# Performance work log

Hardware: AMD Instinct MI355X
Metric: run time of the kernel (lower is better)

The kernel has to match this reference:

```python
import jax, jax.numpy as jnp
import numpy as np
import math

B, S, D = 4, 2048, 1024
TAU = 0.5

def setup_inputs() -> dict:
    key = jax.random.key(0)
    ks = jax.random.split(key, 10)
    s = 1.0 / math.sqrt(D)
    return {
        "node_emb": jax.random.normal(ks[0], (B, S, D), jnp.float32),
        "label_emb": jax.random.normal(ks[1], (B, S, D), jnp.float32),
        "Wq": jax.random.uniform(ks[2], (D, D), jnp.float32, -s, s),
        "bq": jax.random.uniform(ks[3], (D,), jnp.float32, -s, s),
        "Wk": jax.random.uniform(ks[4], (D, D), jnp.float32, -s, s),
        "bk": jax.random.uniform(ks[5], (D,), jnp.float32, -s, s),
        "Wv": jax.random.uniform(ks[6], (D, D), jnp.float32, -s, s),
        "bv": jax.random.uniform(ks[7], (D,), jnp.float32, -s, s),
        "Wp": jax.random.uniform(ks[8], (D, D), jnp.float32, -s, s),
        "bp": jax.random.uniform(ks[9], (D,), jnp.float32, -s, s),
    }

def reference(node_emb, label_emb, Wq, bq, Wk, bk, Wv, bv, Wp, bp):
    # Q from label_emb; K, V from node_emb (torch Linear: x @ W.T + b)
    Q = label_emb @ Wq.T + bq          # [B, S, D]
    K = node_emb @ Wk.T + bk           # [B, S, D]
    V = node_emb @ Wv.T + bv           # [B, S, D]
    d = node_emb.shape[-1]
    score = jnp.einsum('bqd,bkd->bqk', Q, K) / jnp.sqrt(jnp.float32(d))
    # causal (lower-triangular) mask, masked_fill(-1e9) BEFORE the tau scale
    causal = jnp.tril(jnp.ones((score.shape[-2], score.shape[-1]), bool))
    score = jnp.where(causal[None, :, :], score, jnp.float32(-1e9))
    attn = jax.nn.softmax(score * TAU, axis=-1)  # [B, S, S]
    # proj_drop is Dropout(0.1); reference runs in eval mode (identity)
    z = jnp.einsum('bqk,bkd->bqd', attn, V)
    return z @ Wp.T + bp
```

## Files before the change

kernel.cpp:

```cpp
#include <hip/hip_runtime.h>
#include <hip/hip_bf16.h>
#include <stdint.h>

using bf16 = __hip_bfloat16;
typedef __bf16 bf16x8 __attribute__((ext_vector_type(8)));
typedef float f32x4 __attribute__((ext_vector_type(4)));
typedef unsigned short u16x8 __attribute__((ext_vector_type(8)));
typedef unsigned short u16x4 __attribute__((ext_vector_type(4)));

#define AS1 __attribute__((address_space(1)))
#define AS3 __attribute__((address_space(3)))

__device__ inline unsigned short f2b(float f) {
    union { __hip_bfloat16 h; unsigned short u; } cv;
    cv.h = __float2bfloat16(f);
    return cv.u;
}

__global__ __launch_bounds__(256) void cvt6(
    const float* __restrict__ i0, const float* __restrict__ i1,
    const float* __restrict__ i2, const float* __restrict__ i3,
    const float* __restrict__ i4, const float* __restrict__ i5,
    u16x8* __restrict__ o0, u16x8* __restrict__ o1,
    u16x8* __restrict__ o2, u16x8* __restrict__ o3,
    u16x8* __restrict__ o4, u16x8* __restrict__ o5,
    long nbig, long nsmall)
{
    const int y = blockIdx.y;
    const float* in = y == 0 ? i0 : (y == 1 ? i1 : (y == 2 ? i2 : (y == 3 ? i3 : (y == 4 ? i4 : i5))));
    u16x8* out = y == 0 ? o0 : (y == 1 ? o1 : (y == 2 ? o2 : (y == 3 ? o3 : (y == 4 ? o4 : o5))));
    const long n8 = (y < 2) ? nbig : nsmall;
    long i = (long)blockIdx.x * blockDim.x + threadIdx.x;
    const long stride = (long)gridDim.x * blockDim.x;
    const float4* in4 = (const float4*)in;
    for (; i < n8; i += stride) {
        float4 x = in4[2 * i], z = in4[2 * i + 1];
        u16x8 o;
        o[0] = f2b(x.x); o[1] = f2b(x.y); o[2] = f2b(x.z); o[3] = f2b(x.w);
        o[4] = f2b(z.x); o[5] = f2b(z.y); o[6] = f2b(z.z); o[7] = f2b(z.w);
        out[i] = o;
    }
}

template <typename T> __device__ inline void storev(T* p, float v);
template <> __device__ inline void storev<float>(float* p, float v) { *p = v; }
template <> __device__ inline void storev<bf16>(bf16* p, float v) { *p = __float2bfloat16(v); }

template <typename OutT, int MODE>
__global__ __launch_bounds__(512, 2) void gemmX(
    const bf16* __restrict__ A0, const bf16* __restrict__ A1,
    const bf16* __restrict__ B0p, const bf16* __restrict__ B1p,
    OutT* __restrict__ C0, OutT* __restrict__ C1,
    const float* __restrict__ bias0, const float* __restrict__ bias1,
    float scale, int lda, int ldb, int ldc, int Kdim,
    long sA, long sB, long sC)
{
    __shared__ __align__(16) char lds[131072];

    const int nwg = gridDim.x;
    const int bid = blockIdx.x;
    const int s = (nwg & 7) ? bid : ((bid & 7) * (nwg >> 3) + (bid >> 3));

    int bm, ccol0, rowB0, seg = 0, bn_s = 0, zidx = 0;
    const bf16 *A, *B;
    OutT* C;
    const float* bias = nullptr;

    if constexpr (MODE == 0) {
        bm = s >> 3; const int bnl = s & 7; seg = bnl >> 2;
        A = A0; B = B0p; rowB0 = bnl * 256;
        C = seg ? C1 : C0; bias = seg ? bias1 : bias0;
        ccol0 = (bnl & 3) * 256;
    } else if constexpr (MODE == 1) {
        seg = s >> 7; const int r = s & 127; bm = r >> 2; const int bn = r & 3;
        A = seg ? A1 : A0; B = seg ? B1p : B0p;
        C = seg ? C1 : C0; bias = seg ? nullptr : bias0;
        rowB0 = bn * 256; ccol0 = bn * 256;
    } else {
        const int z = s / 36, f = s % 36;
        int m = 0;
        while ((m + 1) * (m + 2) / 2 <= f) ++m;
        bm = m; const int bn = f - m * (m + 1) / 2;
        bn_s = bn; zidx = z;
        A = A0 + (long)z * sA; B = B0p + (long)z * sB; C = C0 + (long)z * sC;
        rowB0 = bn * 256; ccol0 = bn * 256;
    }

    const int KT = Kdim >> 6;
    const int NIT = KT >> 1;

    const int tid = threadIdx.x;
    const int lane = tid & 63;
    const int w = tid >> 6;
    const int wm = w >> 2;
    const int wn = w & 3;

    const int rowA0 = bm * 256;

    const int rr  = tid >> 3;
    const int lch = (tid & 7) ^ (rr & 7);
    const bf16* gAt = A + (long)(rowA0 + rr) * lda + lch * 8;
    const bf16* gBt = B + (long)(rowB0 + rr) * ldb + lch * 8;

#define LA(b) (lds + (b) * 65536)
#define LB(b) (lds + 32768 + (b) * 65536)

    auto SG2 = [&](const bf16* g, int ld, char* dst) {
        __builtin_amdgcn_global_load_lds((const AS1 void*)g,
            (AS3 void*)(dst + tid * 16), 16, 0, 0);
        __builtin_amdgcn_global_load_lds((const AS1 void*)(g + (long)64 * ld),
            (AS3 void*)(dst + 8192 + tid * 16), 16, 0, 0);
    };
    auto ST_A = [&](int kt, int half, int b) {
        SG2(gAt + (long)kt * 64 + (long)half * 128 * lda, lda, LA(b) + half * 16384);
    };
    auto ST_B = [&](int kt, int half, int b) {
        SG2(gBt + (long)kt * 64 + (long)half * 128 * ldb, ldb, LB(b) + half * 16384);
    };

    const int abase = (wm * 128 + (lane & 15)) * 128;
    const int bbase = (wn * 64 + (lane & 15)) * 128;
    const int cc0 = (((lane >> 4) << 4)) ^ ((lane & 7) << 4);
    const int cc1 = cc0 ^ 64;

#define RAF(b, mh, mi, kk) (*(const bf16x8*)(LA(b) + abase + (mh)*8192 + (mi)*2048 + ((kk) ? cc1 : cc0)))
#define RBF(b, ni, kk)     (*(const bf16x8*)(LB(b) + bbase + (ni)*2048 + ((kk) ? cc1 : cc0)))

    f32x4 acc[8][4] = {};
    bf16x8 ar[4][2], blo[2][2], bhi[2][2];

#define RD_A2(b, mh, MI0) { ar[MI0][0] = RAF(b, mh, MI0, 0); ar[MI0][1] = RAF(b, mh, MI0, 1); \
                            ar[(MI0)+1][0] = RAF(b, mh, (MI0)+1, 0); ar[(MI0)+1][1] = RAF(b, mh, (MI0)+1, 1); }
#define RD_BLO(b)   { blo[0][0] = RBF(b, 0, 0); blo[0][1] = RBF(b, 0, 1); blo[1][0] = RBF(b, 1, 0); blo[1][1] = RBF(b, 1, 1); }
#define RD_BHI(b)   { bhi[0][0] = RBF(b, 2, 0); bhi[0][1] = RBF(b, 2, 1); bhi[1][0] = RBF(b, 3, 0); bhi[1][1] = RBF(b, 3, 1); }

#define MQ1(MI, bb, MH, NB) { \
    f32x4 t0_ = acc[(MH)*4 + (MI)][(NB)]; \
    t0_ = __builtin_amdgcn_mfma_f32_16x16x32_bf16(ar[MI][0], bb[0][0], t0_, 0, 0, 0); \
    t0_ = __builtin_amdgcn_mfma_f32_16x16x32_bf16(ar[MI][1], bb[0][1], t0_, 0, 0, 0); \
    acc[(MH)*4 + (MI)][(NB)] = t0_; \
    f32x4 t1_ = acc[(MH)*4 + (MI)][(NB) + 1]; \
    t1_ = __builtin_amdgcn_mfma_f32_16x16x32_bf16(ar[MI][0], bb[1][0], t1_, 0, 0, 0); \
    t1_ = __builtin_amdgcn_mfma_f32_16x16x32_bf16(ar[MI][1], bb[1][1], t1_, 0, 0, 0); \
    acc[(MH)*4 + (MI)][(NB) + 1] = t1_; }

#define SCHEDB     __builtin_amdgcn_sched_barrier(0)
#define PRE_SYNC { asm volatile("s_waitcnt lgkmcnt(0)" ::: "memory"); __builtin_amdgcn_sched_barrier(0); \
                   __builtin_amdgcn_s_barrier(); __builtin_amdgcn_sched_barrier(0); }

    auto BAR = [&]() { __builtin_amdgcn_s_barrier(); SCHEDB; };
    auto PRIO1 = [&]() { __builtin_amdgcn_s_setprio(1); };
    auto PRIO0 = [&]() { __builtin_amdgcn_s_setprio(0); };

    ST_A(0, 0, 0); ST_A(0, 1, 0); ST_B(0, 0, 0); ST_B(0, 1, 0);
    ST_B(1, 0, 1); ST_B(1, 1, 1);
    asm volatile("s_waitcnt vmcnt(4)" ::: "memory");
    BAR();
    RD_BLO(0); RD_A2(0, 0, 0); RD_A2(0, 0, 2);

    for (int i = 0; i < NIT; ++i) {
        const int t0 = 2 * i;
        const bool last = (i == NIT - 1);

        ST_A(t0 + 1, 0, 1);
        PRE_SYNC; PRIO1();
        RD_BHI(0);
        MQ1(0, blo, 0, 0); MQ1(1, blo, 0, 0); MQ1(2, blo, 0, 0); MQ1(3, blo, 0, 0);
        PRIO0();

        ST_A(t0 + 1, 1, 1);
        PRE_SYNC; PRIO1();
        MQ1(0, bhi, 0, 2); MQ1(1, bhi, 0, 2); MQ1(2, bhi, 0, 2); MQ1(3, bhi, 0, 2);
        RD_A2(0, 1, 0); RD_A2(0, 1, 2);
        PRIO0();

        if (!last) ST_B(t0 + 2, 0, 0);
        PRE_SYNC; PRIO1();
        MQ1(0, bhi, 1, 2); MQ1(1, bhi, 1, 2); MQ1(2, bhi, 1, 2); MQ1(3, bhi, 1, 2);
        PRIO0();

        if (!last) { ST_B(t0 + 2, 1, 0);
                     asm volatile("s_waitcnt vmcnt(4)" ::: "memory"); }
        else       { asm volatile("s_waitcnt vmcnt(0)" ::: "memory"); }
        PRE_SYNC; PRIO1();
        MQ1(0, blo, 1, 0); MQ1(1, blo, 1, 0); MQ1(2, blo, 1, 0); MQ1(3, blo, 1, 0);
        RD_BLO(1); RD_A2(1, 0, 0); RD_A2(1, 0, 2);
        PRIO0();

        if (!last) ST_A(t0 + 2, 0, 0);
        PRE_SYNC; PRIO1();
        RD_BHI(1);
        MQ1(0, blo, 0, 0); MQ1(1, blo, 0, 0); MQ1(2, blo, 0, 0); MQ1(3, blo, 0, 0);
        PRIO0();

        if (!last) ST_A(t0 + 2, 1, 0);
        PRE_SYNC; PRIO1();
        MQ1(0, bhi, 0, 2); MQ1(1, bhi, 0, 2); MQ1(2, bhi, 0, 2); MQ1(3, bhi, 0, 2);
        RD_A2(1, 1, 0); RD_A2(1, 1, 2);
        PRIO0();

        if (!last) ST_B(t0 + 3, 0, 1);
        PRE_SYNC; PRIO1();
        MQ1(0, bhi, 1, 2); MQ1(1, bhi, 1, 2); MQ1(2, bhi, 1, 2); MQ1(3, bhi, 1, 2);
        PRIO0();

        if (!last) { ST_B(t0 + 3, 1, 1);
                     asm volatile("s_waitcnt vmcnt(4)" ::: "memory"); }
        PRE_SYNC; PRIO1();
        MQ1(0, blo, 1, 0); MQ1(1, blo, 1, 0); MQ1(2, blo, 1, 0); MQ1(3, blo, 1, 0);
        if (!last) { RD_BLO(0); RD_A2(0, 0, 0); RD_A2(0, 0, 2); }
        PRIO0();
    }

    char* tw = lds + w * 16384;
    if constexpr (MODE == 2) {
        const int q = lane >> 4, t = lane & 15;
        const bool diag = (bm == bn_s);
#pragma unroll
        for (int mi = 0; mi < 8; ++mi)
#pragma unroll
            for (int ni = 0; ni < 4; ++ni)
#pragma unroll
                for (int j = 0; j < 4; ++j) {
                    float e = __expf(acc[mi][ni][j] * scale);
                    if (diag) {
                        const int rl = wm * 128 + mi * 16 + q * 4 + j;
                        const int cl = wn * 64 + t + ni * 16;
                        if (cl > rl) e = 0.f;
                    }
                    e = __bfloat162float(__float2bfloat16(e));
                    acc[mi][ni][j] = e;
                }
        float* part = (float*)C1 + ((((long)zidx * 8 + bm) * 32) + bn_s * 4 + wn) * 256;
#pragma unroll
        for (int mi = 0; mi < 8; ++mi) {
            float rs0 = acc[mi][0][0] + acc[mi][1][0] + acc[mi][2][0] + acc[mi][3][0];
            float rs1 = acc[mi][0][1] + acc[mi][1][1] + acc[mi][2][1] + acc[mi][3][1];
            float rs2 = acc[mi][0][2] + acc[mi][1][2] + acc[mi][2][2] + acc[mi][3][2];
            float rs3 = acc[mi][0][3] + acc[mi][1][3] + acc[mi][2][3] + acc[mi][3][3];
#pragma unroll
            for (int d = 1; d < 16; d <<= 1) {
                rs0 += __shfl_xor(rs0, d); rs1 += __shfl_xor(rs1, d);
                rs2 += __shfl_xor(rs2, d); rs3 += __shfl_xor(rs3, d);
            }
            if (t == mi) {
                float4 o; o.x = rs0; o.y = rs1; o.z = rs2; o.w = rs3;
                *(float4*)(part + wm * 128 + mi * 16 + q * 4) = o;
            }
        }
    }
    if (MODE == 1 && seg == 1) {
#pragma unroll
        for (int ni = 0; ni < 4; ++ni) {
            const int cl = ni * 16 + (lane & 15);
            const int sw = 8 * (cl & 7);
#pragma unroll
            for (int mi = 0; mi < 8; ++mi) {
                const int rlb = mi * 16 + ((lane >> 4) << 2);
                u16x4 o;
                o[0] = f2b(acc[mi][ni][0]); o[1] = f2b(acc[mi][ni][1]);
                o[2] = f2b(acc[mi][ni][2]); o[3] = f2b(acc[mi][ni][3]);
                *(u16x4*)(tw + cl * 256 + 2 * (rlb ^ sw)) = o;
            }
        }
        asm volatile("s_waitcnt lgkmcnt(0)" ::: "memory");
        __builtin_amdgcn_sched_barrier(0);
        const int m0 = rowA0 + wm * 128;
        const int z2 = m0 >> 11, mr = m0 & 2047;
        bf16* CT = (bf16*)C + (long)z2 * 2097152 + (long)(ccol0 + wn * 64 + lane) * 2048 + mr;
        const char* tr = tw + lane * 256;
        const int sw2 = lane & 7;
#pragma unroll
        for (int rb = 0; rb < 16; ++rb) {
            u16x8 v = *(const u16x8*)(tr + 16 * (rb ^ sw2));
            *(u16x8*)(CT + 8 * rb) = v;
        }
    } else {
        const float sc2 = (MODE == 2) ? 1.0f : scale;
        const int q = lane >> 4, t = lane & 15;
        const int c0 = ccol0 + wn * 64 + t;
#pragma unroll
        for (int mi = 0; mi < 8; ++mi) {
            char* tm = tw + mi * 2048;
#pragma unroll
            for (int ni = 0; ni < 4; ++ni) {
                const float bv = bias ? bias[c0 + ni * 16] : 0.0f;
                const int cb = (t + 16 * ni) * 2;
#pragma unroll
                for (int j = 0; j < 4; ++j) {
                    const int rl = q * 4 + j;
                    *(bf16*)(tm + rl * 128 + (cb ^ ((rl & 7) << 4))) =
                        __float2bfloat16(acc[mi][ni][j] * sc2 + bv);
                }
            }
        }
        asm volatile("s_waitcnt lgkmcnt(0)" ::: "memory");
        __builtin_amdgcn_sched_barrier(0);
        const int rr2 = lane >> 2, chb = (lane & 3) * 2;
        const int gr0 = rowA0 + wm * 128;
        bf16* Cb = (bf16*)C;
        const int gcb = ccol0 + wn * 64;
#pragma unroll
        for (int mi = 0; mi < 8; ++mi) {
            const char* tm = tw + mi * 2048;
            const long gr = gr0 + mi * 16 + rr2;
#pragma unroll
            for (int k = 0; k < 2; ++k) {
                const int chunk = chb + k;
                u16x8 v = *(const u16x8*)(tm + rr2 * 128 + ((chunk << 4) ^ ((rr2 & 7) << 4)));
                *(u16x8*)(Cb + gr * (long)ldc + gcb + chunk * 8) = v;
            }
        }
    }
#undef RAF
#undef RBF
#undef RD_A2
#undef RD_BLO
#undef RD_BHI
#undef MQ1
#undef LA
#undef LB
}

__global__ __launch_bounds__(512, 2) void pv_bal(
    const bf16* __restrict__ P, const bf16* __restrict__ VT,
    const float* __restrict__ part, float* __restrict__ out,
    const float* __restrict__ bias)
{
    __shared__ __align__(16) char lds[99328];
    float* invl = (float*)(lds + 98304);

    const int nwg = gridDim.x;
    const int bid = blockIdx.x;
    const int s = (bid & 7) * (nwg >> 3) + (bid >> 3);
    const int z = s >> 6, r = s & 63;
    const int pr = r >> 3, bn = r & 7;
    const int bmA = pr, bmB = 15 - pr;

    const bf16* Pz = P + (long)z * 2048 * 2048;
    const bf16* Vz = VT + (long)z * 1024 * 2048;

    const int tid = threadIdx.x;
    const int lane = tid & 63;
    const int w = tid >> 6;
    const int wm = w >> 2, wn = w & 3;
    const int rr = tid >> 3;
    const int lch = (tid & 7) ^ (rr & 7);

    if (tid < 256) {
        const int half = tid >> 7, rloc = tid & 127;
        const int grow = (half ? bmB : bmA) * 128 + rloc;
        const int b256 = grow >> 8, rin = grow & 255;
        const float* pp = part + (((long)z * 8 + b256) * 32) * 256 + rin;
        const int n4 = 4 * (b256 + 1);
        float s0 = 0.f, s1 = 0.f, s2 = 0.f, s3 = 0.f;
        int b4 = 0;
        for (; b4 + 4 <= n4; b4 += 4) {
            s0 += pp[(long)b4 * 256];       s1 += pp[(long)(b4 + 1) * 256];
            s2 += pp[(long)(b4 + 2) * 256]; s3 += pp[(long)(b4 + 3) * 256];
        }
        for (; b4 < n4; ++b4) s0 += pp[(long)b4 * 256];
        invl[tid] = 1.0f / ((s0 + s1) + (s2 + s3));
    }

    const bf16* gBt = Vz + (long)(bn * 128 + rr) * 2048 + lch * 8;
    const bf16* gAtA = Pz + (long)(bmA * 128 + rr) * 2048 + lch * 8;
    const bf16* gAtB = Pz + (long)(bmB * 128 + rr) * 2048 + lch * 8;

    auto SG2 = [&](const bf16* g, char* dst) {
        __builtin_amdgcn_global_load_lds((const AS1 void*)g,
            (AS3 void*)(dst + tid * 16), 16, 0, 0);
        __builtin_amdgcn_global_load_lds((const AS1 void*)(g + (long)64 * 2048),
            (AS3 void*)(dst + 8192 + tid * 16), 16, 0, 0);
    };
    auto ST = [&](const bf16* gAt, int kt, int b) {
        SG2(gAt + (long)kt * 64, lds + b * 32768);
        SG2(gBt + (long)kt * 64, lds + b * 32768 + 16384);
    };

    const int abase0 = (wm * 64 + (lane & 15)) * 128;
    const int bbase0 = 16384 + (wn * 32 + (lane & 15)) * 128;
    const int cc0 = ((lane >> 4) << 4) ^ ((lane & 7) << 4);
    const int cc1 = cc0 ^ 64;

    f32x4 acc[4][2];
    bf16x8 ar[4][2], br[2][2];

    auto RDF = [&](int t) {
        const char* base = lds + (t % 3) * 32768;
#pragma unroll
        for (int mi = 0; mi < 4; ++mi) {
            ar[mi][0] = *(const bf16x8*)(base + abase0 + mi * 2048 + cc0);
            ar[mi][1] = *(const bf16x8*)(base + abase0 + mi * 2048 + cc1);
        }
#pragma unroll
        for (int ni = 0; ni < 2; ++ni) {
            br[ni][0] = *(const bf16x8*)(base + bbase0 + ni * 2048 + cc0);
            br[ni][1] = *(const bf16x8*)(base + bbase0 + ni * 2048 + cc1);
        }
    };
    auto MFMA16 = [&]() {
#pragma unroll
        for (int mi = 0; mi < 4; ++mi)
#pragma unroll
            for (int ni = 0; ni < 2; ++ni) {
                f32x4 t_ = acc[mi][ni];
                t_ = __builtin_amdgcn_mfma_f32_16x16x32_bf16(ar[mi][0], br[ni][0], t_, 0, 0, 0);
                t_ = __builtin_amdgcn_mfma_f32_16x16x32_bf16(ar[mi][1], br[ni][1], t_, 0, 0, 0);
                acc[mi][ni] = t_;
            }
    };
    auto ZERO = [&]() {
#pragma unroll
        for (int mi = 0; mi < 4; ++mi)
#pragma unroll
            for (int ni = 0; ni < 2; ++ni) acc[mi][ni] = f32x4{0.f, 0.f, 0.f, 0.f};
    };
    auto tile_pass = [&](const bf16* gAt, int KT) {
        RDF(0);
        for (int t = 0; t < KT; ++t) {
            if (t + 2 < KT) {
                ST(gAt, t + 2, (t + 2) % 3);
                asm volatile("s_waitcnt vmcnt(4)" ::: "memory");
            } else if (t + 1 < KT) {
                asm volatile("s_waitcnt vmcnt(0)" ::: "memory");
            }
            asm volatile("s_waitcnt lgkmcnt(0)" ::: "memory");
            __builtin_amdgcn_sched_barrier(0);
            __builtin_amdgcn_s_barrier();
            __builtin_amdgcn_sched_barrier(0);
            __builtin_amdgcn_s_setprio(1);
            MFMA16();
            if (t + 1 < KT) RDF(t + 1);
            __builtin_amdgcn_s_setprio(0);
        }
    };
    auto epi = [&](int bm, int invoff) {
        const int q = lane >> 4, t16 = lane & 15;
        const int c0 = bn * 128 + wn * 32 + t16;
        float* op = out + ((long)z * 2048 + (long)bm * 128) * 1024;
#pragma unroll
        for (int mi = 0; mi < 4; ++mi)
#pragma unroll
            for (int j = 0; j < 4; ++j) {
                const int rl = wm * 64 + mi * 16 + q * 4 + j;
                const float iv = invl[invoff + rl];
#pragma unroll
                for (int ni = 0; ni < 2; ++ni) {
                    const int c = c0 + ni * 16;
                    op[(long)rl * 1024 + c] = acc[mi][ni][j] * iv + bias[c];
                }
            }
    };

    const int KTA = 2 * (bmA + 1), KTB = 2 * (bmB + 1);

    ST(gAtA, 0, 0); ST(gAtA, 1, 1);
    asm volatile("s_waitcnt vmcnt(4)" ::: "memory");
    __builtin_amdgcn_s_barrier();
    __builtin_amdgcn_sched_barrier(0);
    ZERO();
    tile_pass(gAtA, KTA);

    ST(gAtB, 0, 0); ST(gAtB, 1, 1);
    epi(bmA, 0);
    asm volatile("s_waitcnt vmcnt(0)" ::: "memory");
    __builtin_amdgcn_s_barrier();
    __builtin_amdgcn_sched_barrier(0);
    ZERO();
    tile_pass(gAtB, KTB);
    epi(bmB, 128);
}

extern "C" void kernel_launch(void* const* d_in, const int* in_sizes, int n_in,
                              void* d_out, int out_size, void* d_ws, size_t ws_size,
                              hipStream_t stream) {
    const int B = 4, S = 2048, D = 1024;
    const long MD = (long)B * S * D;
    const float scale = 0.5f / 32.0f;

    const float* node  = (const float*)d_in[0];
    const float* label = (const float*)d_in[1];
    const float* Wq = (const float*)d_in[2];
    const float* bq = (const float*)d_in[3];
    const float* Wk = (const float*)d_in[4];
    const float* bk = (const float*)d_in[5];
    const float* Wv = (const float*)d_in[6];
    const float* bv = (const float*)d_in[7];
    const float* Wp = (const float*)d_in[8];
    const float* bp = (const float*)d_in[9];
    float* out = (float*)d_out;

    char* ws = (char*)d_ws;
    bf16* nodeb  = (bf16*)(ws);
    bf16* VTb    = nodeb;
    bf16* labelb = (bf16*)(ws + 16777216);
    bf16* Wqb = (bf16*)(ws + 33554432);
    bf16* Wkb = (bf16*)(ws + 35651584);
    bf16* Wvb = (bf16*)(ws + 37748736);
    bf16* Wpb = (bf16*)(ws + 39845888);
    bf16* Qb  = (bf16*)(ws + 41943040);
    bf16* Kb  = (bf16*)(ws + 58720256);
    bf16* Vb  = (bf16*)(ws + 75497472);
    float* partial = (float*)(ws + 75497472);
    bf16* SP  = (bf16*)(ws + 92274688);
    if (ws_size < 125829120UL) return;

    cvt6<<<dim3(512, 6), 256, 0, stream>>>(
        node, label, Wq, Wk, Wv, Wp,
        (u16x8*)nodeb, (u16x8*)labelb, (u16x8*)Wqb, (u16x8*)Wkb, (u16x8*)Wvb, (u16x8*)Wpb,
        MD / 8, (long)D * D / 8);

    gemmX<bf16, 0><<<256, 512, 0, stream>>>(
        nodeb, nullptr, Wkb, nullptr, Kb, Vb, bk, bv,
        1.0f, D, D, D, D, 0, 0, 0);

    gemmX<bf16, 1><<<256, 512, 0, stream>>>(
        labelb, Vb, Wqb, Wpb, Qb, VTb, bq, nullptr,
        1.0f, D, D, D, D, 0, 0, 0);

    gemmX<bf16, 2><<<144, 512, 0, stream>>>(
        Qb, nullptr, Kb, (bf16*)nullptr, SP, (bf16*)partial, nullptr, nullptr,
        scale, D, D, S, D, (long)S * D, (long)S * D, (long)S * S);

    pv_bal<<<256, 512, 0, stream>>>(SP, VTb, partial, out, bp);
}
```

Baseline: 153.4 us.

## Double-buffer GEMM fragment registers and drop per-phase lgkmcnt waits

Restructures the GEMM main loop's LDS-to-register schedule. A fragments now use separate even and odd register sets, and B-low fragments are double-buffered across k-tiles. The explicit lgkmcnt(0) waits before each barrier are removed, so LDS reads can overlap the MFMA phases and waits are left to the compiler. This raises VGPR pressure and relies on the compiler inserting correct waits; B-high fragments are no longer double-buffered, so the reordering has to keep reads ahead of the async global-to-LDS overwrites.

```diff
diff --git a/kernel.cpp b/kernel.cpp
--- a/kernel.cpp
+++ b/kernel.cpp
@@ -127,89 +127,78 @@
 #define RBF(b, ni, kk)     (*(const bf16x8*)(LB(b) + bbase + (ni)*2048 + ((kk) ? cc1 : cc0)))
 
     f32x4 acc[8][4] = {};
-    bf16x8 ar[4][2], blo[2][2], bhi[2][2];
-
-#define RD_A2(b, mh, MI0) { ar[MI0][0] = RAF(b, mh, MI0, 0); ar[MI0][1] = RAF(b, mh, MI0, 1); \
-                            ar[(MI0)+1][0] = RAF(b, mh, (MI0)+1, 0); ar[(MI0)+1][1] = RAF(b, mh, (MI0)+1, 1); }
-#define RD_BLO(b)   { blo[0][0] = RBF(b, 0, 0); blo[0][1] = RBF(b, 0, 1); blo[1][0] = RBF(b, 1, 0); blo[1][1] = RBF(b, 1, 1); }
-#define RD_BHI(b)   { bhi[0][0] = RBF(b, 2, 0); bhi[0][1] = RBF(b, 2, 1); bhi[1][0] = RBF(b, 3, 0); bhi[1][1] = RBF(b, 3, 1); }
-
-#define MQ1(MI, bb, MH, NB) { \
-    f32x4 t0_ = acc[(MH)*4 + (MI)][(NB)]; \
-    t0_ = __builtin_amdgcn_mfma_f32_16x16x32_bf16(ar[MI][0], bb[0][0], t0_, 0, 0, 0); \
-    t0_ = __builtin_amdgcn_mfma_f32_16x16x32_bf16(ar[MI][1], bb[0][1], t0_, 0, 0, 0); \
-    acc[(MH)*4 + (MI)][(NB)] = t0_; \
-    f32x4 t1_ = acc[(MH)*4 + (MI)][(NB) + 1]; \
-    t1_ = __builtin_amdgcn_mfma_f32_16x16x32_bf16(ar[MI][0], bb[1][0], t1_, 0, 0, 0); \
-    t1_ = __builtin_amdgcn_mfma_f32_16x16x32_bf16(ar[MI][1], bb[1][1], t1_, 0, 0, 0); \
-    acc[(MH)*4 + (MI)][(NB) + 1] = t1_; }
-
-#define SCHEDB     __builtin_amdgcn_sched_barrier(0)
-#define PRE_SYNC { asm volatile("s_waitcnt lgkmcnt(0)" ::: "memory"); __builtin_amdgcn_sched_barrier(0); \
-                   __builtin_amdgcn_s_barrier(); __builtin_amdgcn_sched_barrier(0); }
-
-    auto BAR = [&]() { __builtin_amdgcn_s_barrier(); SCHEDB; };
+    bf16x8 arE[4][2], arO[4][2], blA[2][2], blB[2][2], bh[2][2];
+
+#define RD_AE(b) { _Pragma("unroll") for (int mi = 0; mi < 4; ++mi) { arE[mi][0] = RAF(b, 0, mi, 0); arE[mi][1] = RAF(b, 0, mi, 1); } }
+#define RD_AO(b) { _Pragma("unroll") for (int mi = 0; mi < 4; ++mi) { arO[mi][0] = RAF(b, 1, mi, 0); arO[mi][1] = RAF(b, 1, mi, 1); } }
+#define RD_BLX(b, dst) { dst[0][0] = RBF(b, 0, 0); dst[0][1] = RBF(b, 0, 1); dst[1][0] = RBF(b, 1, 0); dst[1][1] = RBF(b, 1, 1); }
+#define RD_BHX(b)      { bh[0][0] = RBF(b, 2, 0); bh[0][1] = RBF(b, 2, 1); bh[1][0] = RBF(b, 3, 0); bh[1][1] = RBF(b, 3, 1); }
+
+#define MQX(ASET, BSET, MH, NB) { \
+    _Pragma("unroll") \
+    for (int mi = 0; mi < 4; ++mi) { \
+        f32x4 t0_ = acc[(MH)*4 + mi][(NB)]; \
+        t0_ = __builtin_amdgcn_mfma_f32_16x16x32_bf16(ASET[mi][0], BSET[0][0], t0_, 0, 0, 0); \
+        t0_ = __builtin_amdgcn_mfma_f32_16x16x32_bf16(ASET[mi][1], BSET[0][1], t0_, 0, 0, 0); \
+        acc[(MH)*4 + mi][(NB)] = t0_; \
+        f32x4 t1_ = acc[(MH)*4 + mi][(NB) + 1]; \
+        t1_ = __builtin_amdgcn_mfma_f32_16x16x32_bf16(ASET[mi][0], BSET[1][0], t1_, 0, 0, 0); \
+        t1_ = __builtin_amdgcn_mfma_f32_16x16x32_bf16(ASET[mi][1], BSET[1][1], t1_, 0, 0, 0); \
+        acc[(MH)*4 + mi][(NB) + 1] = t1_; } }
+
+#define SCHEDB __builtin_amdgcn_sched_barrier(0)
+#define BARX   { __builtin_amdgcn_s_barrier(); SCHEDB; }
+#define VM4    { asm volatile("s_waitcnt vmcnt(4)" ::: "memory"); SCHEDB; }
+#define VM0    { asm volatile("s_waitcnt vmcnt(0)" ::: "memory"); SCHEDB; }
+
     auto PRIO1 = [&]() { __builtin_amdgcn_s_setprio(1); };
     auto PRIO0 = [&]() { __builtin_amdgcn_s_setprio(0); };
 
     ST_A(0, 0, 0); ST_A(0, 1, 0); ST_B(0, 0, 0); ST_B(0, 1, 0);
     ST_B(1, 0, 1); ST_B(1, 1, 1);
-    asm volatile("s_waitcnt vmcnt(4)" ::: "memory");
-    BAR();
-    RD_BLO(0); RD_A2(0, 0, 0); RD_A2(0, 0, 2);
+    VM4; BARX;
+    RD_AE(0); RD_BLX(0, blA); RD_BHX(0);
 
     for (int i = 0; i < NIT; ++i) {
         const int t0 = 2 * i;
         const bool last = (i == NIT - 1);
 
         ST_A(t0 + 1, 0, 1);
-        PRE_SYNC; PRIO1();
-        RD_BHI(0);
-        MQ1(0, blo, 0, 0); MQ1(1, blo, 0, 0); MQ1(2, blo, 0, 0); MQ1(3, blo, 0, 0);
-        PRIO0();
+        BARX;
+        RD_AO(0);
+        PRIO1(); MQX(arE, blA, 0, 0); PRIO0();
 
         ST_A(t0 + 1, 1, 1);
-        PRE_SYNC; PRIO1();
-        MQ1(0, bhi, 0, 2); MQ1(1, bhi, 0, 2); MQ1(2, bhi, 0, 2); MQ1(3, bhi, 0, 2);
-        RD_A2(0, 1, 0); RD_A2(0, 1, 2);
-        PRIO0();
-
+        BARX;
+        PRIO1(); MQX(arE, bh, 0, 2); PRIO0();
+
+        BARX;
         if (!last) ST_B(t0 + 2, 0, 0);
-        PRE_SYNC; PRIO1();
-        MQ1(0, bhi, 1, 2); MQ1(1, bhi, 1, 2); MQ1(2, bhi, 1, 2); MQ1(3, bhi, 1, 2);
-        PRIO0();
-
-        if (!last) { ST_B(t0 + 2, 1, 0);
-                     asm volatile("s_waitcnt vmcnt(4)" ::: "memory"); }
-        else       { asm volatile("s_waitcnt vmcnt(0)" ::: "memory"); }
-        PRE_SYNC; PRIO1();
-        MQ1(0, blo, 1, 0); MQ1(1, blo, 1, 0); MQ1(2, blo, 1, 0); MQ1(3, blo, 1, 0);
-        RD_BLO(1); RD_A2(1, 0, 0); RD_A2(1, 0, 2);
-        PRIO0();
+        PRIO1(); MQX(arO, bh, 1, 2); PRIO0();
+
+        if (!last) { ST_B(t0 + 2, 1, 0); VM4; }
+        else       { VM0; }
+        BARX;
+        RD_AE(1); RD_BLX(1, blB); RD_BHX(1);
+        PRIO1(); MQX(arO, blA, 1, 0); PRIO0();
 
         if (!last) ST_A(t0 + 2, 0, 0);
-        PRE_SYNC; PRIO1();
-        RD_BHI(1);
-        MQ1(0, blo, 0, 0); MQ1(1, blo, 0, 0); MQ1(2, blo, 0, 0); MQ1(3, blo, 0, 0);
-        PRIO0();
+        BARX;
+        RD_AO(1);
+        PRIO1(); MQX(arE, blB, 0, 0); PRIO0();
 
         if (!last) ST_A(t0 + 2, 1, 0);
-        PRE_SYNC; PRIO1();
-        MQ1(0, bhi, 0, 2); MQ1(1, bhi, 0, 2); MQ1(2, bhi, 0, 2); MQ1(3, bhi, 0, 2);
-        RD_A2(1, 1, 0); RD_A2(1, 1, 2);
-        PRIO0();
-
+        BARX;
+        PRIO1(); MQX(arE, bh, 0, 2); PRIO0();
+
+        BARX;
         if (!last) ST_B(t0 + 3, 0, 1);
-        PRE_SYNC; PRIO1();
-        MQ1(0, bhi, 1, 2); MQ1(1, bhi, 1, 2); MQ1(2, bhi, 1, 2); MQ1(3, bhi, 1, 2);
-        PRIO0();
-
-        if (!last) { ST_B(t0 + 3, 1, 1);
-                     asm volatile("s_waitcnt vmcnt(4)" ::: "memory"); }
-        PRE_SYNC; PRIO1();
-        MQ1(0, blo, 1, 0); MQ1(1, blo, 1, 0); MQ1(2, blo, 1, 0); MQ1(3, blo, 1, 0);
-        if (!last) { RD_BLO(0); RD_A2(0, 0, 0); RD_A2(0, 0, 2); }
-        PRIO0();
+        PRIO1(); MQX(arO, bh, 1, 2); PRIO0();
+
+        if (!last) { ST_B(t0 + 3, 1, 1); VM4; }
+        BARX;
+        if (!last) { RD_AE(0); RD_BLX(0, blA); RD_BHX(0); }
+        PRIO1(); MQX(arO, blB, 1, 0); PRIO0();
     }
 
     char* tw = lds + w * 16384;
@@ -314,10 +303,11 @@
     }
 #undef RAF
 #undef RBF
-#undef RD_A2
-#undef RD_BLO
-#undef RD_BHI
-#undef MQ1
+#undef RD_AE
+#undef RD_AO
+#undef RD_BLX
+#undef RD_BHX
+#undef MQX
 #undef LA
 #undef LB
 }
```

New measurement: 269.8 us. +75.9%, slower.
